# Performance work log

Measured on AMD Instinct MI355X. Metric: run time of the kernel, lower is better.

Reference implementation:

```python
import jax, jax.numpy as jnp
import numpy as np

EPS = 1e-8


def _similarity(feat):
    # feat: [b, c, h, w] -> pixel-pair cosine-similarity matrix [b, hw, hw]
    b, c, h, w = feat.shape
    feat = feat.astype(jnp.float32)
    # channel-wise L2 norm per pixel, eps added AFTER sqrt (matches torch code)
    norm = jnp.sqrt(jnp.sum(feat * feat, axis=1, keepdims=True)) + EPS  # [b,1,h,w]
    f = (feat / norm).reshape(b, c, h * w)                              # [b,c,hw]
    return jnp.einsum('icm,icn->imn', f, f)                             # [b,hw,hw]


def _sim_distance(feat1, feat2):
    b, _, h, w = feat1.shape
    hw = h * w
    sim_err = (_similarity(feat1) - _similarity(feat2)) ** 2 / (hw * hw) / b
    return jnp.sum(sim_err)


def setup_inputs() -> dict:
    key = jax.random.key(0)
    k1, k2, k3, k4 = jax.random.split(key, 4)
    return {
        'res1_t': jax.random.normal(k1, (4, 128, 64, 64), dtype=jnp.float32),
        'res1_s': jax.random.normal(k2, (4, 128, 64, 64), dtype=jnp.float32),
        'res2_t': jax.random.normal(k3, (4, 256, 32, 32), dtype=jnp.float32),
        'res2_s': jax.random.normal(k4, (4, 256, 32, 32), dtype=jnp.float32),
    }


def reference(res1_t, res1_s, res2_t, res2_s):
    # teacher features are detached in the original; forward math is identical
    pwl_g1 = _sim_distance(res1_t, res1_s)
    pwl_g2 = _sim_distance(res2_t, res2_s)
    loss = pwl_g1 + pwl_g2
    return (loss, jnp.stack([loss, pwl_g1, pwl_g2]))
```

## Files before the change

### kernel.cpp

```cpp
#include <hip/hip_runtime.h>
#include <math.h>

#define EPSF 1e-8f

typedef __attribute__((ext_vector_type(4))) short short4v;
typedef __attribute__((ext_vector_type(8))) short short8v;
typedef __attribute__((ext_vector_type(4))) float float4v;

__device__ inline short f2bf(float f) {
    unsigned u = __builtin_bit_cast(unsigned, f);
    unsigned r = (u + 0x7FFFu + ((u >> 16) & 1u)) >> 16;
    return (short)r;
}
__device__ inline float bf2f(short s) {
    unsigned u = ((unsigned)(unsigned short)s) << 16;
    return __builtin_bit_cast(float, u);
}

#define F1T 0
#define F1S 2097152
#define F2T 4194304
#define F2S 5242880

__constant__ int g2q_tab[10][4] = {
    {0,0,0,1},{0,0,1,2},{0,1,1,1},
    {1,0,0,1},{1,0,1,2},{1,1,1,1},
    {2,0,0,-2},{2,0,1,-2},{2,1,0,-2},{2,1,1,-2},
};

template<int C, int HW>
__device__ inline void prep_body(const float* __restrict__ x,
                                 short* __restrict__ f, int lp, int t)
{
    const int lanei = t & 7, slice = t >> 3;
    const int b = lp / HW, m = lp - b * HW;
    const float* p = x + (size_t)b * C * HW + m;
    short*       q = f + (size_t)b * C * HW + m;
    constexpr int CPR = C >> 5;
    short4v vals[CPR];
    float4 s0 = {0.f,0.f,0.f,0.f}, s1 = {0.f,0.f,0.f,0.f};
#pragma unroll
    for (int i = 0; i < CPR; i += 2) {
        float4 v0 = *(const float4*)(p + (size_t)(slice * CPR + i)     * HW);
        float4 v1 = *(const float4*)(p + (size_t)(slice * CPR + i + 1) * HW);
        s0.x += v0.x * v0.x; s0.y += v0.y * v0.y;
        s0.z += v0.z * v0.z; s0.w += v0.w * v0.w;
        s1.x += v1.x * v1.x; s1.y += v1.y * v1.y;
        s1.z += v1.z * v1.z; s1.w += v1.w * v1.w;
        vals[i]     = (short4v){ f2bf(v0.x), f2bf(v0.y), f2bf(v0.z), f2bf(v0.w) };
        vals[i + 1] = (short4v){ f2bf(v1.x), f2bf(v1.y), f2bf(v1.z), f2bf(v1.w) };
    }
    float4 s = { s0.x + s1.x, s0.y + s1.y, s0.z + s1.z, s0.w + s1.w };
    __shared__ float4 red[32][8];
    __shared__ float4 invl[8];
    red[slice][lanei] = s;
    __syncthreads();
    if (t < 8) {
        float4 tot = {0.f,0.f,0.f,0.f};
#pragma unroll
        for (int sl = 0; sl < 32; ++sl) {
            float4 v = red[sl][t];
            tot.x += v.x; tot.y += v.y; tot.z += v.z; tot.w += v.w;
        }
        invl[t] = (float4){ 1.f / (sqrtf(tot.x) + EPSF), 1.f / (sqrtf(tot.y) + EPSF),
                            1.f / (sqrtf(tot.z) + EPSF), 1.f / (sqrtf(tot.w) + EPSF) };
    }
    __syncthreads();
    const float4 iv = invl[lanei];
#pragma unroll
    for (int i = 0; i < CPR; ++i) {
        const int r = slice * CPR + i;
        short4v rv = vals[i];
        short4v o = { f2bf(bf2f(rv[0]) * iv.x), f2bf(bf2f(rv[1]) * iv.y),
                      f2bf(bf2f(rv[2]) * iv.z), f2bf(bf2f(rv[3]) * iv.w) };
        *(short4v*)(q + (size_t)r * HW) = o;
    }
}

__global__ __launch_bounds__(256) void prep_kernel(
    const float* __restrict__ x1t, const float* __restrict__ x1s,
    const float* __restrict__ x2t, const float* __restrict__ x2s,
    short* __restrict__ F, float* __restrict__ out,
    unsigned* __restrict__ cnt)
{
    const int gp = blockIdx.x * 32;
    const int t = threadIdx.x;
    const int lanei = t & 7;
    if (blockIdx.x == 0 && t < 4) out[t] = 0.f;
    if (blockIdx.x == 0 && t == 4) *cnt = 0u;
    if (gp < 16384)
        prep_body<128, 4096>(x1t, F + F1T, gp + lanei * 4, t);
    else if (gp < 32768)
        prep_body<128, 4096>(x1s, F + F1S, gp - 16384 + lanei * 4, t);
    else if (gp < 36864)
        prep_body<256, 1024>(x2t, F + F2T, gp - 32768 + lanei * 4, t);
    else
        prep_body<256, 1024>(x2s, F + F2S, gp - 36864 + lanei * 4, t);
}

#define ASTR 72

template<int HW, bool SHARE>
__device__ inline void gram_tile128(const short* __restrict__ Fa,
                                    const short* __restrict__ Fb,
                                    int k0, int t,
                                    short* __restrict__ ldsA,
                                    short* __restrict__ ldsB,
                                    float4v (&acc)[4][4])
{
    const int lane = t & 63, w = t >> 6;
    const int r16 = lane & 15, quad = lane >> 4;
    const int wr = w >> 1, wc = w & 1;
    const int srow = t >> 3, skc = (t & 7) * 8;

    short8v ar[4], br[4];
#pragma unroll
    for (int p = 0; p < 4; ++p)
        ar[p] = *(const short8v*)(Fa + (size_t)(p * 32 + srow) * HW + k0 + skc);
    if (!SHARE) {
#pragma unroll
        for (int p = 0; p < 4; ++p)
            br[p] = *(const short8v*)(Fb + (size_t)(p * 32 + srow) * HW + k0 + skc);
    }

#pragma unroll 1
    for (int st = 0; st < 8; ++st) {
#pragma unroll
        for (int p = 0; p < 4; ++p)
            *(short8v*)(ldsA + (p * 32 + srow) * ASTR + skc) = ar[p];
        if (!SHARE) {
#pragma unroll
            for (int p = 0; p < 4; ++p)
                *(short8v*)(ldsB + (p * 32 + srow) * ASTR + skc) = br[p];
        }
        __syncthreads();
        if (st < 7) {
            const int k1 = k0 + (st + 1) * 64;
#pragma unroll
            for (int p = 0; p < 4; ++p)
                ar[p] = *(const short8v*)(Fa + (size_t)(p * 32 + srow) * HW + k1 + skc);
            if (!SHARE) {
#pragma unroll
                for (int p = 0; p < 4; ++p)
                    br[p] = *(const short8v*)(Fb + (size_t)(p * 32 + srow) * HW + k1 + skc);
            }
        }
        const short* A = ldsA;
        const short* B = SHARE ? ldsA : ldsB;
#pragma unroll
        for (int ks = 0; ks < 2; ++ks) {
            short8v af[4], bf[4];
#pragma unroll
            for (int i = 0; i < 4; ++i)
                af[i] = *(const short8v*)(A + (wr * 64 + i * 16 + r16) * ASTR + ks * 32 + quad * 8);
#pragma unroll
            for (int j = 0; j < 4; ++j)
                bf[j] = *(const short8v*)(B + (wc * 64 + j * 16 + r16) * ASTR + ks * 32 + quad * 8);
#pragma unroll
            for (int i = 0; i < 4; ++i)
#pragma unroll
                for (int j = 0; j < 4; ++j)
                    acc[i][j] = __builtin_amdgcn_mfma_f32_16x16x32_bf16(
                        af[i], bf[j], acc[i][j], 0, 0, 0);
        }
        __syncthreads();
    }
}

__global__ __launch_bounds__(256, 2) void gram_kernel(
    const short* __restrict__ F, float* __restrict__ partials)
{
    __shared__ __align__(16) short ldsA[128 * ASTR];
    __shared__ __align__(16) short ldsB[128 * ASTR];

    const int id = blockIdx.x;
    const int t = threadIdx.x, w = t >> 6, lane = t & 63;
    const int r16 = lane & 15, quad = lane >> 4;
    const int wr = w >> 1, wc = w & 1;

    float4v acc[4][4];
#pragma unroll
    for (int i = 0; i < 4; ++i)
#pragma unroll
        for (int j = 0; j < 4; ++j) acc[i][j] = (float4v){0.f, 0.f, 0.f, 0.f};

    int slab;
    if (id < 96) {
        const int jb = id >> 3, ks = id & 7;
        const int type = jb >> 2, b = jb & 3;
        const int k0 = ks * 512;
        const short* Fa = (type == 1 ? F + F1S : F + F1T) + (size_t)b * 524288;
        const short* Fb = (type == 0 ? F + F1T : F + F1S) + (size_t)b * 524288;
        if (type < 2) gram_tile128<4096, true >(Fa, Fa, k0, t, ldsA, ldsB, acc);
        else          gram_tile128<4096, false>(Fa, Fb, k0, t, ldsA, ldsB, acc);
        slab = jb * 8 + ks;
    } else {
        const int id2 = id - 96;
        const int job = id2 >> 1, ks = id2 & 1;
        const int b = job / 10, j10 = job - b * 10;
        const int type = g2q_tab[j10][0];
        const int qi = g2q_tab[j10][1], qj = g2q_tab[j10][2];
        const int k0 = ks * 512;
        const short* Fa = (type == 1 ? F + F2S : F + F2T)
                          + (size_t)(b * 256 + qi * 128) * 1024;
        const short* Fb = (type == 0 ? F + F2T : F + F2S)
                          + (size_t)(b * 256 + qj * 128) * 1024;
        if (type < 2 && qi == qj)
            gram_tile128<1024, true >(Fa, Fa, k0, t, ldsA, ldsB, acc);
        else
            gram_tile128<1024, false>(Fa, Fb, k0, t, ldsA, ldsB, acc);
        slab = 96 + job * 2 + ks;
    }

    float* dst = partials + (size_t)slab * 16384;
#pragma unroll
    for (int i = 0; i < 4; ++i)
#pragma unroll
        for (int j = 0; j < 4; ++j)
#pragma unroll
            for (int r = 0; r < 4; ++r)
                dst[(wr * 64 + i * 16 + quad * 4 + r) * 128 + wc * 64 + j * 16 + r16]
                    = acc[i][j][r];
}

template<int P>
__device__ inline float fin_sum(const float* __restrict__ base, int part, int t)
{
    float s = 0.f;
    const int off = part * 4096 + t * 4;
#pragma unroll
    for (int i = 0; i < 4; ++i) {
        const int idx = off + i * 1024;
        float4 v = {0.f, 0.f, 0.f, 0.f};
#pragma unroll
        for (int p = 0; p < P; ++p) {
            float4 u = *(const float4*)(base + (size_t)p * 16384 + idx);
            v.x += u.x; v.y += u.y; v.z += u.z; v.w += u.w;
        }
        s += v.x * v.x + v.y * v.y + v.z * v.z + v.w * v.w;
    }
    return s;
}

__global__ __launch_bounds__(256) void fin_kernel(
    const float* __restrict__ partials, float* __restrict__ out,
    unsigned* __restrict__ cnt)
{
    __shared__ float sc[4];
    const int bid = blockIdx.x;
    const int t = threadIdx.x, lane = t & 63, w = t >> 6;

    float s, wt; int which;
    if (bid < 48) {
        const int tile = bid >> 2, part = bid & 3;
        const int type = tile >> 2;
        s = fin_sum<8>(partials + (size_t)tile * 8 * 16384, part, t);
        wt = (type == 2 ? -2.f : 1.f) * (1.0f / (4096.f * 4096.f * 4.f));
        which = 2;
    } else {
        const int b2 = bid - 48;
        const int job = b2 >> 2, part = b2 & 3;
        const int j10 = job % 10;
        s = fin_sum<2>(partials + (size_t)(96 + job * 2) * 16384, part, t);
        wt = (float)g2q_tab[j10][3] * (1.0f / (1024.f * 1024.f * 4.f));
        which = 3;
    }
    s *= wt;

#pragma unroll
    for (int o = 32; o > 0; o >>= 1) s += __shfl_down(s, o);
    if (lane == 0) sc[w] = s;
    __syncthreads();
    if (t == 0) {
        float val = sc[0] + sc[1] + sc[2] + sc[3];
        atomicAdd(&out[which], val);
        __threadfence();
        unsigned old = atomicAdd(cnt, 1u);
        if (old == 207u) {
            float g1v = __hip_atomic_load(&out[2], __ATOMIC_RELAXED,
                                          __HIP_MEMORY_SCOPE_AGENT);
            float g2v = __hip_atomic_load(&out[3], __ATOMIC_RELAXED,
                                          __HIP_MEMORY_SCOPE_AGENT);
            float loss = g1v + g2v;
            out[0] = loss;
            out[1] = loss;
        }
    }
}

extern "C" void kernel_launch(void* const* d_in, const int* in_sizes, int n_in,
                              void* d_out, int out_size, void* d_ws, size_t ws_size,
                              hipStream_t stream)
{
    const float* x1t = (const float*)d_in[0];
    const float* x1s = (const float*)d_in[1];
    const float* x2t = (const float*)d_in[2];
    const float* x2s = (const float*)d_in[3];

    short* F        = (short*)d_ws;
    float* partials = (float*)d_ws + 3200000;
    unsigned* cnt   = (unsigned*)((float*)d_ws + 6200000);

    prep_kernel<<<1280, 256, 0, stream>>>(x1t, x1s, x2t, x2s, F,
                                          (float*)d_out, cnt);
    gram_kernel<<<176, 256, 0, stream>>>(F, partials);
    fin_kernel<<<208, 256, 0, stream>>>(partials, (float*)d_out, cnt);
}
```

Before: 94.58 us.

## Double split-K block count and double-buffer global loads in gram tile

Each gram block now covers 256 of the K dimension instead of 512, so the grid grows from 176 to 352 blocks and more of the GPU's compute units are occupied. The tile loop is fully unrolled to four steps with two register buffers, so global loads are issued two stages ahead. The finish kernel now reduces twice as many partial slabs, and the counter is moved in the workspace to make room for them. This trades more partial-sum memory traffic and a larger reduction for better occupancy and more latency hiding.

Result: no change. 95.46 us (+0.9%).

```diff
diff --git a/kernel.cpp b/kernel.cpp
--- a/kernel.cpp
+++ b/kernel.cpp
@@ -113,38 +113,29 @@
     const int wr = w >> 1, wc = w & 1;
     const int srow = t >> 3, skc = (t & 7) * 8;
 
-    short8v ar[4], br[4];
-#pragma unroll
-    for (int p = 0; p < 4; ++p)
-        ar[p] = *(const short8v*)(Fa + (size_t)(p * 32 + srow) * HW + k0 + skc);
-    if (!SHARE) {
+    short8v arA[4], brA[4], arB[4], brB[4];
+
+    auto loadA = [&](short8v (&ra)[4], short8v (&rb)[4], int kk) {
 #pragma unroll
         for (int p = 0; p < 4; ++p)
-            br[p] = *(const short8v*)(Fb + (size_t)(p * 32 + srow) * HW + k0 + skc);
-    }
-
-#pragma unroll 1
-    for (int st = 0; st < 8; ++st) {
+            ra[p] = *(const short8v*)(Fa + (size_t)(p * 32 + srow) * HW + kk + skc);
+        if (!SHARE) {
+#pragma unroll
+            for (int p = 0; p < 4; ++p)
+                rb[p] = *(const short8v*)(Fb + (size_t)(p * 32 + srow) * HW + kk + skc);
+        }
+    };
+    auto store = [&](short8v (&ra)[4], short8v (&rb)[4]) {
 #pragma unroll
         for (int p = 0; p < 4; ++p)
-            *(short8v*)(ldsA + (p * 32 + srow) * ASTR + skc) = ar[p];
+            *(short8v*)(ldsA + (p * 32 + srow) * ASTR + skc) = ra[p];
         if (!SHARE) {
 #pragma unroll
             for (int p = 0; p < 4; ++p)
-                *(short8v*)(ldsB + (p * 32 + srow) * ASTR + skc) = br[p];
-        }
-        __syncthreads();
-        if (st < 7) {
-            const int k1 = k0 + (st + 1) * 64;
-#pragma unroll
-            for (int p = 0; p < 4; ++p)
-                ar[p] = *(const short8v*)(Fa + (size_t)(p * 32 + srow) * HW + k1 + skc);
-            if (!SHARE) {
-#pragma unroll
-                for (int p = 0; p < 4; ++p)
-                    br[p] = *(const short8v*)(Fb + (size_t)(p * 32 + srow) * HW + k1 + skc);
-            }
-        }
+                *(short8v*)(ldsB + (p * 32 + srow) * ASTR + skc) = rb[p];
+        }
+    };
+    auto compute = [&]() {
         const short* A = ldsA;
         const short* B = SHARE ? ldsA : ldsB;
 #pragma unroll
@@ -163,8 +154,22 @@
                     acc[i][j] = __builtin_amdgcn_mfma_f32_16x16x32_bf16(
                         af[i], bf[j], acc[i][j], 0, 0, 0);
         }
-        __syncthreads();
-    }
+    };
+
+    loadA(arA, brA, k0);
+    loadA(arB, brB, k0 + 64);
+
+    store(arA, brA); __syncthreads();
+    loadA(arA, brA, k0 + 128);
+    compute(); __syncthreads();
+    store(arB, brB); __syncthreads();
+    loadA(arB, brB, k0 + 192);
+    compute(); __syncthreads();
+    store(arA, brA); __syncthreads();
+    compute(); __syncthreads();
+    store(arB, brB); __syncthreads();
+    compute();
+    __syncthreads();
 }
 
 __global__ __launch_bounds__(256, 2) void gram_kernel(
@@ -184,23 +189,21 @@
 #pragma unroll
         for (int j = 0; j < 4; ++j) acc[i][j] = (float4v){0.f, 0.f, 0.f, 0.f};
 
-    int slab;
-    if (id < 96) {
-        const int jb = id >> 3, ks = id & 7;
+    if (id < 192) {
+        const int jb = id >> 4, ks = id & 15;
         const int type = jb >> 2, b = jb & 3;
-        const int k0 = ks * 512;
+        const int k0 = ks * 256;
         const short* Fa = (type == 1 ? F + F1S : F + F1T) + (size_t)b * 524288;
         const short* Fb = (type == 0 ? F + F1T : F + F1S) + (size_t)b * 524288;
         if (type < 2) gram_tile128<4096, true >(Fa, Fa, k0, t, ldsA, ldsB, acc);
         else          gram_tile128<4096, false>(Fa, Fb, k0, t, ldsA, ldsB, acc);
-        slab = jb * 8 + ks;
     } else {
-        const int id2 = id - 96;
-        const int job = id2 >> 1, ks = id2 & 1;
+        const int id2 = id - 192;
+        const int job = id2 >> 2, ks = id2 & 3;
         const int b = job / 10, j10 = job - b * 10;
         const int type = g2q_tab[j10][0];
         const int qi = g2q_tab[j10][1], qj = g2q_tab[j10][2];
-        const int k0 = ks * 512;
+        const int k0 = ks * 256;
         const short* Fa = (type == 1 ? F + F2S : F + F2T)
                           + (size_t)(b * 256 + qi * 128) * 1024;
         const short* Fb = (type == 0 ? F + F2T : F + F2S)
@@ -209,10 +212,9 @@
             gram_tile128<1024, true >(Fa, Fa, k0, t, ldsA, ldsB, acc);
         else
             gram_tile128<1024, false>(Fa, Fb, k0, t, ldsA, ldsB, acc);
-        slab = 96 + job * 2 + ks;
-    }
-
-    float* dst = partials + (size_t)slab * 16384;
+    }
+
+    float* dst = partials + (size_t)id * 16384;
 #pragma unroll
     for (int i = 0; i < 4; ++i)
 #pragma unroll
@@ -254,14 +256,14 @@
     if (bid < 48) {
         const int tile = bid >> 2, part = bid & 3;
         const int type = tile >> 2;
-        s = fin_sum<8>(partials + (size_t)tile * 8 * 16384, part, t);
+        s = fin_sum<16>(partials + (size_t)tile * 16 * 16384, part, t);
         wt = (type == 2 ? -2.f : 1.f) * (1.0f / (4096.f * 4096.f * 4.f));
         which = 2;
     } else {
         const int b2 = bid - 48;
         const int job = b2 >> 2, part = b2 & 3;
         const int j10 = job % 10;
-        s = fin_sum<2>(partials + (size_t)(96 + job * 2) * 16384, part, t);
+        s = fin_sum<4>(partials + (size_t)(192 + job * 4) * 16384, part, t);
         wt = (float)g2q_tab[j10][3] * (1.0f / (1024.f * 1024.f * 4.f));
         which = 3;
     }
@@ -299,10 +301,10 @@
 
     short* F        = (short*)d_ws;
     float* partials = (float*)d_ws + 3200000;
-    unsigned* cnt   = (unsigned*)((float*)d_ws + 6200000);
+    unsigned* cnt   = (unsigned*)((float*)d_ws + 9000000);
 
     prep_kernel<<<1280, 256, 0, stream>>>(x1t, x1s, x2t, x2s, F,
                                           (float*)d_out, cnt);
-    gram_kernel<<<176, 256, 0, stream>>>(F, partials);
+    gram_kernel<<<352, 256, 0, stream>>>(F, partials);
     fin_kernel<<<208, 256, 0, stream>>>(partials, (float*)d_out, cnt);
 }
```
